# Kernel optimization log

Hardware: AMD Instinct MI355X
Metric: run time of the kernel (lower is better)

Reference implementation:

```python
import math
import jax, jax.numpy as jnp
import numpy as np

B, L, DM, H = 4, 1024, 1024, 16
D = DM // H  # head dim = 64
MAXPOS = 1024


def setup_inputs() -> dict:
    key = jax.random.key(0)
    ks = jax.random.split(key, 8)
    s = 0.02
    return {
        "hidden_states": jax.random.normal(ks[0], (B, L, DM), jnp.float32),
        "attention_mask": jnp.zeros((B, 1, 1, L), jnp.float32),
        "Wq": jax.random.normal(ks[1], (DM, DM), jnp.float32) * s,
        "bq": jax.random.normal(ks[2], (DM,), jnp.float32) * s,
        "Wk": jax.random.normal(ks[3], (DM, DM), jnp.float32) * s,
        "bk": jax.random.normal(ks[4], (DM,), jnp.float32) * s,
        "Wv": jax.random.normal(ks[5], (DM, DM), jnp.float32) * s,
        "bv": jax.random.normal(ks[6], (DM,), jnp.float32) * s,
        "dist_emb": jax.random.normal(ks[7], (2 * MAXPOS - 1, D), jnp.float32) * s,
    }


def reference(hidden_states, attention_mask, Wq, bq, Wk, bk, Wv, bv, dist_emb):
    b, l, dm = hidden_states.shape

    def split_heads(x):  # [b,l,dm] -> [b,h,l,d]
        return x.reshape(b, l, H, D).transpose(0, 2, 1, 3)

    # nn.Linear applies x @ W.T + b
    q = split_heads(hidden_states @ Wq.T + bq)
    k = split_heads(hidden_states @ Wk.T + bk)
    v = split_heads(hidden_states @ Wv.T + bv)

    scores = jnp.einsum("bhld,bhrd->bhlr", q, k)

    # relative_key_query positional bias
    pos = jnp.arange(l)
    idx = pos[:, None] - pos[None, :] + MAXPOS - 1  # [l,l] in [0, 2*MAXPOS-2]
    pe = dist_emb[idx]  # [l,l,d]
    scores = scores + jnp.einsum("bhld,lrd->bhlr", q, pe) \
                    + jnp.einsum("bhrd,lrd->bhlr", k, pe)

    scores = scores / math.sqrt(D) + attention_mask
    probs = jax.nn.softmax(scores, axis=-1)  # dropout p=0.0 -> identity

    ctx = jnp.einsum("bhlr,bhrd->bhld", probs, v)
    return ctx.transpose(0, 2, 1, 3).reshape(b, l, dm)
```

## Files before the change

### kernel.cpp

```cpp
#include <hip/hip_runtime.h>

typedef __attribute__((ext_vector_type(4))) float f32x4;
typedef __attribute__((ext_vector_type(8))) short short8;
typedef __attribute__((ext_vector_type(2))) unsigned u32x2;

typedef __attribute__((address_space(1))) const void gv_t;
typedef __attribute__((address_space(3))) void lv_t;

__device__ __forceinline__ ushort f2bf(float f) {
  union { float f; unsigned u; } v; v.f = f;
  unsigned r = v.u + 0x7fffu + ((v.u >> 16) & 1u);
  return (ushort)(r >> 16);
}
__device__ __forceinline__ float bf2f(ushort u) {
  union { unsigned u; float f; } v; v.u = ((unsigned)u) << 16;
  return v.f;
}

template<int CTRL>
__device__ __forceinline__ float dppf(float x) {
  union { float f; int i; } u; u.f = x;
  u.i = __builtin_amdgcn_update_dpp(0, u.i, CTRL, 0xf, 0xf, true);
  return u.f;
}
__device__ __forceinline__ float rmax16(float x) {
  x = fmaxf(x, dppf<0xB1>(x));
  x = fmaxf(x, dppf<0x4E>(x));
  x = fmaxf(x, dppf<0x124>(x));
  x = fmaxf(x, dppf<0x128>(x));
  return x;
}
__device__ __forceinline__ float rsum16(float x) {
  x += dppf<0xB1>(x);
  x += dppf<0x4E>(x);
  x += dppf<0x124>(x);
  x += dppf<0x128>(x);
  return x;
}

__global__ void k_prep(const float* __restrict__ hidden, const float* __restrict__ Wq,
                       const float* __restrict__ Wk, const float* __restrict__ Wv,
                       const float* __restrict__ dist, const float* __restrict__ bq,
                       const float* __restrict__ bk, const float* __restrict__ bv,
                       ushort* __restrict__ Hbf, ushort* __restrict__ Wqkv,
                       ushort* __restrict__ Ebf, float* __restrict__ Bqkv) {
  int i = blockIdx.x * blockDim.x + threadIdx.x;
  const float* src; ushort* dst; int o;
  if (i < 1048576)      { src = hidden; o = i;            dst = Hbf; }
  else if (i < 1310720) { src = Wq;   o = i - 1048576;    dst = Wqkv; }
  else if (i < 1572864) { src = Wk;   o = i - 1310720;    dst = Wqkv + 1048576; }
  else if (i < 1835008) { src = Wv;   o = i - 1572864;    dst = Wqkv + 2097152; }
  else if (i < 1867760) { src = dist; o = i - 1835008;    dst = Ebf; }
  else if (i < 1868528) {
    int ib = i - 1867760;
    const float* bs = ib < 256 ? bq : (ib < 512 ? bk : bv);
    reinterpret_cast<float4*>(Bqkv)[ib] = reinterpret_cast<const float4*>(bs)[ib & 255];
    return;
  } else return;
  float4 v = reinterpret_cast<const float4*>(src)[o];
  ushort4 u;
  u.x = f2bf(v.x); u.y = f2bf(v.y); u.z = f2bf(v.z); u.w = f2bf(v.w);
  reinterpret_cast<ushort4*>(dst)[o] = u;
}

__global__ __launch_bounds__(256) void k_gemm_qkv(
    const ushort* __restrict__ A, const ushort* __restrict__ W,
    const float* __restrict__ bias, ushort* __restrict__ C)
{
  __shared__ __align__(16) ushort As[128 * 32];
  __shared__ __align__(16) ushort Bs[128 * 32];
  const int n0 = blockIdx.x * 128;
  const int m0 = blockIdx.y * 128;
  const int tid = threadIdx.x;
  const int w = tid >> 6, lane = tid & 63;
  const int wr = (w >> 1) * 64, wc = (w & 1) * 64;
  const int lr = lane & 15, lk = (lane >> 4) * 8;

  f32x4 acc[4][4] = {};

  for (int k0 = 0; k0 < 1024; k0 += 32) {
    __syncthreads();
#pragma unroll
    for (int inst = 0; inst < 2; ++inst) {
      int chunk = w * 128 + inst * 64 + lane;
      int row = chunk >> 2, c8 = (chunk & 3) * 8;
      __builtin_amdgcn_global_load_lds(
          (gv_t*)(A + (size_t)(m0 + row) * 1024 + k0 + c8),
          (lv_t*)(As + (size_t)(w * 128 + inst * 64) * 8), 16, 0, 0);
      __builtin_amdgcn_global_load_lds(
          (gv_t*)(W + (size_t)(n0 + row) * 1024 + k0 + c8),
          (lv_t*)(Bs + (size_t)(w * 128 + inst * 64) * 8), 16, 0, 0);
    }
    __syncthreads();
    short8 af[4], bfr[4];
#pragma unroll
    for (int t = 0; t < 4; ++t) {
      af[t]  = *reinterpret_cast<const short8*>(As + (wr + t * 16 + lr) * 32 + lk);
      bfr[t] = *reinterpret_cast<const short8*>(Bs + (wc + t * 16 + lr) * 32 + lk);
    }
#pragma unroll
    for (int mt = 0; mt < 4; ++mt)
#pragma unroll
      for (int nt = 0; nt < 4; ++nt)
        acc[mt][nt] = __builtin_amdgcn_mfma_f32_16x16x32_bf16(af[mt], bfr[nt], acc[mt][nt], 0, 0, 0);
  }

  float bv[4];
#pragma unroll
  for (int nt = 0; nt < 4; ++nt) bv[nt] = bias[n0 + wc + nt * 16 + lr];
#pragma unroll
  for (int mt = 0; mt < 4; ++mt)
#pragma unroll
    for (int nt = 0; nt < 4; ++nt)
#pragma unroll
      for (int j = 0; j < 4; ++j) {
        int row = m0 + wr + mt * 16 + (lane >> 4) * 4 + j;
        int col = n0 + wc + nt * 16 + lr;
        C[(size_t)row * 3072 + col] = f2bf(acc[mt][nt][j] + bv[nt]);
      }
}

__global__ __launch_bounds__(256) void k_vt(const ushort* __restrict__ QKV,
                                            ushort* __restrict__ VT) {
  __shared__ ushort t[64][65];
  const int bh = blockIdx.y, b = bh >> 4, h = bh & 15;
  const int l0 = blockIdx.x * 64;
  const int r = threadIdx.x >> 2, c0 = (threadIdx.x & 3) * 16;
  const ushort* src = QKV + (size_t)(b * 1024 + l0 + r) * 3072 + 2048 + h * 64 + c0;
  short8 v0 = *reinterpret_cast<const short8*>(src);
  short8 v1 = *reinterpret_cast<const short8*>(src + 8);
#pragma unroll
  for (int i = 0; i < 8; ++i) {
    t[c0 + i][r] = (ushort)v0[i];
    t[c0 + 8 + i][r] = (ushort)v1[i];
  }
  __syncthreads();
  short8 o0, o1;
#pragma unroll
  for (int i = 0; i < 8; ++i) {
    o0[i] = (short)t[r][c0 + i];
    o1[i] = (short)t[r][c0 + 8 + i];
  }
  ushort* dst = VT + (size_t)(bh * 64 + r) * 1024 + l0 + c0;
  *reinterpret_cast<short8*>(dst) = o0;
  *reinterpret_cast<short8*>(dst + 8) = o1;
}

__global__ __launch_bounds__(512, 4) void k_attn(
    const ushort* __restrict__ QKV, const ushort* __restrict__ VTg,
    const ushort* __restrict__ E, const float* __restrict__ mask,
    float* __restrict__ out)
{
  __shared__ __align__(16) ushort Kl[64 * 64];
  __shared__ __align__(16) ushort Vl[64 * 64];
  __shared__ __align__(16) ushort El[256 * 64];
  __shared__ __align__(16) ushort T2s[64 * 196];

  const int lt = blockIdx.x, h = blockIdx.y, b = blockIdx.z;
  const int bh = b * 16 + h;
  const int l0 = lt * 128;
  const int tid = threadIdx.x;
  const int w = tid >> 6, lane = tid & 63;
  const int g = lane >> 4, m = lane & 15, g4 = g * 4;
  const int rsub = lane >> 3, csub = lane & 7;

  const ushort* Qg = QKV;
  const ushort* Kg = QKV + 1024;
  const float* maskrow = mask + b * 1024;

  short8 qf0, qf1;
  {
    const size_t qoff = (size_t)(b * 1024 + l0 + w * 16 + m) * 3072 + h * 64;
    qf0 = *reinterpret_cast<const short8*>(Qg + qoff + g * 8);
    qf1 = *reinterpret_cast<const short8*>(Qg + qoff + 32 + g * 8);
  }

  int srcl[4], bsel[4];
#pragma unroll
  for (int j = 0; j < 4; ++j) {
    int x = (g4 + j + 63 - m) & 15;
    srcl[j] = (lane & 48) | x;
    bsel[j] = (g4 + j) > x;
  }
  const int A0 = 195 * m + 16 * w + g4 + 63;
  const int tile0 = (w < 4) ? 2 * w : 4 + w;

  {
    int kr = w * 8 + rsub;
    __builtin_amdgcn_global_load_lds(
        (gv_t*)(Kg + (size_t)(b * 1024 + kr) * 3072 + h * 64 + ((csub ^ (kr & 7)) << 3)),
        (lv_t*)(Kl + w * 512), 16, 0, 0);
#pragma unroll
    for (int i = 0; i < 3; ++i) {
      int li = w * 3 + i;
      int er = li * 8 + rsub;
      int p = l0 + 960 + er; if (p > 2046) p = 2046;
      __builtin_amdgcn_global_load_lds(
          (gv_t*)(E + (size_t)p * 64 + ((csub ^ (er & 7)) << 3)),
          (lv_t*)(El + li * 512), 16, 0, 0);
    }
  }

  f32x4 o_[4] = {};
  float m_[4], s_[4];
#pragma unroll
  for (int j = 0; j < 4; ++j) { m_[j] = -1e30f; s_[j] = 0.f; }

  int rot = 0;

  for (int rt = 0; rt < 16; ++rt) {
    const int r0 = rt * 64;
    __syncthreads();

    {
      int dr = w * 8 + rsub;
      __builtin_amdgcn_global_load_lds(
          (gv_t*)(VTg + (size_t)(bh * 64 + dr) * 1024 + r0 + ((csub ^ (dr & 7)) << 3)),
          (lv_t*)(Vl + w * 512), 16, 0, 0);
    }

    short8 ea0[2], ea1[2];
    {
      int row = tile0 * 16 + m, phys = (row + rot) & 255;
      ea0[0] = *reinterpret_cast<const short8*>(El + phys * 64 + ((g ^ (row & 7)) << 3));
      ea0[1] = *reinterpret_cast<const short8*>(El + phys * 64 + (((g + 4) ^ (row & 7)) << 3));
    }
    if (w < 4) {
      int row = (tile0 + 1) * 16 + m, phys = (row + rot) & 255;
      ea1[0] = *reinterpret_cast<const short8*>(El + phys * 64 + ((g ^ (row & 7)) << 3));
      ea1[1] = *reinterpret_cast<const short8*>(El + phys * 64 + (((g + 4) ^ (row & 7)) << 3));
    }

    f32x4 sc[4];
#pragma unroll
    for (int ft = 0; ft < 4; ++ft) {
      int kr = ft * 16 + m;
      short8 kb0 = *reinterpret_cast<const short8*>(Kl + kr * 64 + ((g ^ (kr & 7)) << 3));
      short8 kb1 = *reinterpret_cast<const short8*>(Kl + kr * 64 + (((g + 4) ^ (kr & 7)) << 3));
      f32x4 z = {0.f, 0.f, 0.f, 0.f};
      sc[ft] = __builtin_amdgcn_mfma_f32_16x16x32_bf16(qf1, kb1,
               __builtin_amdgcn_mfma_f32_16x16x32_bf16(qf0, kb0, z, 0, 0, 0), 0, 0, 0);
      {
        f32x4 t2 = __builtin_amdgcn_mfma_f32_16x16x32_bf16(ea0[1], kb1,
                   __builtin_amdgcn_mfma_f32_16x16x32_bf16(ea0[0], kb0, z, 0, 0, 0), 0, 0, 0);
        u32x2 pk;
        pk[0] = (unsigned)f2bf(t2[0]) | ((unsigned)f2bf(t2[1]) << 16);
        pk[1] = (unsigned)f2bf(t2[2]) | ((unsigned)f2bf(t2[3]) << 16);
        *reinterpret_cast<u32x2*>(T2s + (ft * 16 + m) * 196 + tile0 * 16 + g4) = pk;
      }
      if (w < 4) {
        f32x4 t2 = __builtin_amdgcn_mfma_f32_16x16x32_bf16(ea1[1], kb1,
                   __builtin_amdgcn_mfma_f32_16x16x32_bf16(ea1[0], kb0, z, 0, 0, 0), 0, 0, 0);
        u32x2 pk;
        pk[0] = (unsigned)f2bf(t2[0]) | ((unsigned)f2bf(t2[1]) << 16);
        pk[1] = (unsigned)f2bf(t2[2]) | ((unsigned)f2bf(t2[3]) << 16);
        *reinterpret_cast<u32x2*>(T2s + (ft * 16 + m) * 196 + (tile0 + 1) * 16 + g4) = pk;
      }
    }

    f32x4 t1loc[5];
#pragma unroll
    for (int lti = 0; lti < 5; ++lti) {
      int row = (w + lti) * 16 + m, phys = (row + rot) & 255;
      short8 e0 = *reinterpret_cast<const short8*>(El + phys * 64 + ((g ^ (row & 7)) << 3));
      short8 e1 = *reinterpret_cast<const short8*>(El + phys * 64 + (((g + 4) ^ (row & 7)) << 3));
      f32x4 z = {0.f, 0.f, 0.f, 0.f};
      t1loc[lti] = __builtin_amdgcn_mfma_f32_16x16x32_bf16(qf1, e1,
                   __builtin_amdgcn_mfma_f32_16x16x32_bf16(qf0, e0, z, 0, 0, 0), 0, 0, 0);
    }

    __syncthreads();

    if (rt < 15) {
      int kr = w * 8 + rsub;
      __builtin_amdgcn_global_load_lds(
          (gv_t*)(Kg + (size_t)(b * 1024 + r0 + 64 + kr) * 3072 + h * 64 + ((csub ^ (kr & 7)) << 3)),
          (lv_t*)(Kl + w * 512), 16, 0, 0);
      int X = (rot + 192) & 255;
      int er = w * 8 + rsub;
      int p = l0 + 960 - 64 * (rt + 1) + er;
      __builtin_amdgcn_global_load_lds(
          (gv_t*)(E + (size_t)p * 64 + ((csub ^ (er & 7)) << 3)),
          (lv_t*)(El + (X + w * 8) * 64), 16, 0, 0);
    }

    float sv[4][4];
#pragma unroll
    for (int ct = 0; ct < 4; ++ct) {
      float mk = maskrow[r0 + ct * 16 + m];
#pragma unroll
      for (int j = 0; j < 4; ++j) {
        float t2v = bf2f(T2s[A0 + 3120 * ct + j]);
        float val = bsel[j] ? t1loc[4 - ct][j] : t1loc[3 - ct][j];
        float t1v = __shfl(val, srcl[j]);
        sv[ct][j] = (sc[ct][j] + t1v + t2v) * 0.125f + mk;
      }
    }

#pragma unroll
    for (int j = 0; j < 4; ++j) {
      float rm = fmaxf(fmaxf(sv[0][j], sv[1][j]), fmaxf(sv[2][j], sv[3][j]));
      rm = rmax16(rm);
      float mn = fmaxf(m_[j], rm);
      float al = __expf(m_[j] - mn);
      float rs = 0.f;
#pragma unroll
      for (int ct = 0; ct < 4; ++ct) {
        float p = __expf(sv[ct][j] - mn);
        sv[ct][j] = p; rs += p;
      }
      rs = rsum16(rs);
      s_[j] = s_[j] * al + rs;
      m_[j] = mn;
#pragma unroll
      for (int vt = 0; vt < 4; ++vt) o_[vt][j] *= al;
    }

    __syncthreads();

    ushort* Pp = (ushort*)T2s;
#pragma unroll
    for (int ct = 0; ct < 4; ++ct)
#pragma unroll
      for (int j = 0; j < 4; ++j) {
        int e = g4 + j;
        int f = ct * 16 + m;
        Pp[w * 1024 + e * 64 + ((((f >> 3) ^ (e & 7)) << 3) | (f & 7))] = f2bf(sv[ct][j]);
      }

    {
      short8 pf0 = *reinterpret_cast<const short8*>(Pp + w * 1024 + m * 64 + ((g ^ (m & 7)) << 3));
      short8 pf1 = *reinterpret_cast<const short8*>(Pp + w * 1024 + m * 64 + (((g + 4) ^ (m & 7)) << 3));
#pragma unroll
      for (int vt = 0; vt < 4; ++vt) {
        int dr = vt * 16 + m;
        short8 vb0 = *reinterpret_cast<const short8*>(Vl + dr * 64 + ((g ^ (dr & 7)) << 3));
        short8 vb1 = *reinterpret_cast<const short8*>(Vl + dr * 64 + (((g + 4) ^ (dr & 7)) << 3));
        o_[vt] = __builtin_amdgcn_mfma_f32_16x16x32_bf16(pf0, vb0, o_[vt], 0, 0, 0);
        o_[vt] = __builtin_amdgcn_mfma_f32_16x16x32_bf16(pf1, vb1, o_[vt], 0, 0, 0);
      }
    }

    rot = (rot + 192) & 255;
  }

#pragma unroll
  for (int j = 0; j < 4; ++j) {
    float inv = 1.0f / s_[j];
    int row = b * 1024 + l0 + w * 16 + g4 + j;
#pragma unroll
    for (int vt = 0; vt < 4; ++vt)
      out[(size_t)row * 1024 + h * 64 + vt * 16 + m] = o_[vt][j] * inv;
  }
}

extern "C" void kernel_launch(void* const* d_in, const int* in_sizes, int n_in,
                              void* d_out, int out_size, void* d_ws, size_t ws_size,
                              hipStream_t stream) {
  const float* hidden = (const float*)d_in[0];
  const float* mask   = (const float*)d_in[1];
  const float* Wq = (const float*)d_in[2];
  const float* bq = (const float*)d_in[3];
  const float* Wk = (const float*)d_in[4];
  const float* bk = (const float*)d_in[5];
  const float* Wv = (const float*)d_in[6];
  const float* bv = (const float*)d_in[7];
  const float* dist = (const float*)d_in[8];
  float* out = (float*)d_out;

  char* ws = (char*)d_ws;
  ushort* Hbf  = (ushort*)(ws);
  ushort* Wqkv = (ushort*)(ws + 8388608);
  float*  Bqkv = (float*) (ws + 8388608 + 6291456);
  ushort* Ebf  = (ushort*)(ws + 8388608 + 6291456 + 16384);
  ushort* QKV  = (ushort*)(ws + 8388608 + 6291456 + 16384 + 262144);
  ushort* VT   = Hbf;

  k_prep<<<7299, 256, 0, stream>>>(hidden, Wq, Wk, Wv, dist, bq, bk, bv,
                                   Hbf, Wqkv, Ebf, Bqkv);
  k_gemm_qkv<<<dim3(24, 32), 256, 0, stream>>>(Hbf, Wqkv, Bqkv, QKV);
  k_vt<<<dim3(16, 64), 256, 0, stream>>>(QKV, VT);
  k_attn<<<dim3(8, 16, 4), 512, 0, stream>>>(QKV, VT, Ebf, mask, out);
}
```

Before: 163.1 us.

## Swizzle block order, shrink E ring buffer, dedicate P buffer, add setprio around MFMAs

```diff
diff --git a/kernel.cpp b/kernel.cpp
--- a/kernel.cpp
+++ b/kernel.cpp
@@ -69,8 +69,10 @@
 {
   __shared__ __align__(16) ushort As[128 * 32];
   __shared__ __align__(16) ushort Bs[128 * 32];
-  const int n0 = blockIdx.x * 128;
-  const int m0 = blockIdx.y * 128;
+  int linear = blockIdx.x + blockIdx.y * 24;
+  int swzb = (linear & 7) * 96 + (linear >> 3);
+  const int n0 = (swzb % 24) * 128;
+  const int m0 = (swzb / 24) * 128;
   const int tid = threadIdx.x;
   const int w = tid >> 6, lane = tid & 63;
   const int wr = (w >> 1) * 64, wc = (w & 1) * 64;
@@ -153,10 +155,14 @@
 {
   __shared__ __align__(16) ushort Kl[64 * 64];
   __shared__ __align__(16) ushort Vl[64 * 64];
-  __shared__ __align__(16) ushort El[256 * 64];
-  __shared__ __align__(16) ushort T2s[64 * 196];
-
-  const int lt = blockIdx.x, h = blockIdx.y, b = blockIdx.z;
+  __shared__ __align__(16) ushort El[192 * 64];
+  __shared__ __align__(16) ushort T2s[64 * 192];
+  __shared__ __align__(16) ushort Pp[8 * 1024];
+
+  int linear = blockIdx.x + (blockIdx.y << 3) + (blockIdx.z << 7);
+  int swzb = (linear & 7) * 64 + (linear >> 3);
+  const int lt = swzb & 7, h = (swzb >> 3) & 15, b = swzb >> 7;
+
   const int bh = b * 16 + h;
   const int l0 = lt * 128;
   const int tid = threadIdx.x;
@@ -182,7 +188,7 @@
     srcl[j] = (lane & 48) | x;
     bsel[j] = (g4 + j) > x;
   }
-  const int A0 = 195 * m + 16 * w + g4 + 63;
+  const int A0 = 191 * m + 16 * w + g4 + 63;
   const int tile0 = (w < 4) ? 2 * w : 4 + w;
 
   {
@@ -221,15 +227,19 @@
 
     short8 ea0[2], ea1[2];
     {
-      int row = tile0 * 16 + m, phys = (row + rot) & 255;
-      ea0[0] = *reinterpret_cast<const short8*>(El + phys * 64 + ((g ^ (row & 7)) << 3));
-      ea0[1] = *reinterpret_cast<const short8*>(El + phys * 64 + (((g + 4) ^ (row & 7)) << 3));
+      int row = tile0 * 16 + m;
+      int x = row + rot; if (x >= 192) x -= 192;
+      ea0[0] = *reinterpret_cast<const short8*>(El + x * 64 + ((g ^ (row & 7)) << 3));
+      ea0[1] = *reinterpret_cast<const short8*>(El + x * 64 + (((g + 4) ^ (row & 7)) << 3));
     }
     if (w < 4) {
-      int row = (tile0 + 1) * 16 + m, phys = (row + rot) & 255;
-      ea1[0] = *reinterpret_cast<const short8*>(El + phys * 64 + ((g ^ (row & 7)) << 3));
-      ea1[1] = *reinterpret_cast<const short8*>(El + phys * 64 + (((g + 4) ^ (row & 7)) << 3));
-    }
+      int row = (tile0 + 1) * 16 + m;
+      int x = row + rot; if (x >= 192) x -= 192;
+      ea1[0] = *reinterpret_cast<const short8*>(El + x * 64 + ((g ^ (row & 7)) << 3));
+      ea1[1] = *reinterpret_cast<const short8*>(El + x * 64 + (((g + 4) ^ (row & 7)) << 3));
+    }
+
+    __builtin_amdgcn_s_setprio(1);
 
     f32x4 sc[4];
 #pragma unroll
@@ -246,7 +256,7 @@
         u32x2 pk;
         pk[0] = (unsigned)f2bf(t2[0]) | ((unsigned)f2bf(t2[1]) << 16);
         pk[1] = (unsigned)f2bf(t2[2]) | ((unsigned)f2bf(t2[3]) << 16);
-        *reinterpret_cast<u32x2*>(T2s + (ft * 16 + m) * 196 + tile0 * 16 + g4) = pk;
+        *reinterpret_cast<u32x2*>(T2s + (ft * 16 + m) * 192 + tile0 * 16 + g4) = pk;
       }
       if (w < 4) {
         f32x4 t2 = __builtin_amdgcn_mfma_f32_16x16x32_bf16(ea1[1], kb1,
@@ -254,21 +264,24 @@
         u32x2 pk;
         pk[0] = (unsigned)f2bf(t2[0]) | ((unsigned)f2bf(t2[1]) << 16);
         pk[1] = (unsigned)f2bf(t2[2]) | ((unsigned)f2bf(t2[3]) << 16);
-        *reinterpret_cast<u32x2*>(T2s + (ft * 16 + m) * 196 + (tile0 + 1) * 16 + g4) = pk;
+        *reinterpret_cast<u32x2*>(T2s + (ft * 16 + m) * 192 + (tile0 + 1) * 16 + g4) = pk;
       }
     }
 
     f32x4 t1loc[5];
 #pragma unroll
     for (int lti = 0; lti < 5; ++lti) {
-      int row = (w + lti) * 16 + m, phys = (row + rot) & 255;
-      short8 e0 = *reinterpret_cast<const short8*>(El + phys * 64 + ((g ^ (row & 7)) << 3));
-      short8 e1 = *reinterpret_cast<const short8*>(El + phys * 64 + (((g + 4) ^ (row & 7)) << 3));
+      int row = (w + lti) * 16 + m;
+      int x = row + rot; if (x >= 192) x -= 192;
+      short8 e0 = *reinterpret_cast<const short8*>(El + x * 64 + ((g ^ (row & 7)) << 3));
+      short8 e1 = *reinterpret_cast<const short8*>(El + x * 64 + (((g + 4) ^ (row & 7)) << 3));
       f32x4 z = {0.f, 0.f, 0.f, 0.f};
       t1loc[lti] = __builtin_amdgcn_mfma_f32_16x16x32_bf16(qf1, e1,
                    __builtin_amdgcn_mfma_f32_16x16x32_bf16(qf0, e0, z, 0, 0, 0), 0, 0, 0);
     }
 
+    __builtin_amdgcn_s_setprio(0);
+
     __syncthreads();
 
     if (rt < 15) {
@@ -276,7 +289,7 @@
       __builtin_amdgcn_global_load_lds(
           (gv_t*)(Kg + (size_t)(b * 1024 + r0 + 64 + kr) * 3072 + h * 64 + ((csub ^ (kr & 7)) << 3)),
           (lv_t*)(Kl + w * 512), 16, 0, 0);
-      int X = (rot + 192) & 255;
+      int X = rot + 128; if (X >= 192) X -= 192;
       int er = w * 8 + rsub;
       int p = l0 + 960 - 64 * (rt + 1) + er;
       __builtin_amdgcn_global_load_lds(
@@ -290,7 +303,7 @@
       float mk = maskrow[r0 + ct * 16 + m];
 #pragma unroll
       for (int j = 0; j < 4; ++j) {
-        float t2v = bf2f(T2s[A0 + 3120 * ct + j]);
+        float t2v = bf2f(T2s[A0 + 3056 * ct + j]);
         float val = bsel[j] ? t1loc[4 - ct][j] : t1loc[3 - ct][j];
         float t1v = __shfl(val, srcl[j]);
         sv[ct][j] = (sc[ct][j] + t1v + t2v) * 0.125f + mk;
@@ -316,9 +329,6 @@
       for (int vt = 0; vt < 4; ++vt) o_[vt][j] *= al;
     }
 
-    __syncthreads();
-
-    ushort* Pp = (ushort*)T2s;
 #pragma unroll
     for (int ct = 0; ct < 4; ++ct)
 #pragma unroll
@@ -331,6 +341,7 @@
     {
       short8 pf0 = *reinterpret_cast<const short8*>(Pp + w * 1024 + m * 64 + ((g ^ (m & 7)) << 3));
       short8 pf1 = *reinterpret_cast<const short8*>(Pp + w * 1024 + m * 64 + (((g + 4) ^ (m & 7)) << 3));
+      __builtin_amdgcn_s_setprio(1);
 #pragma unroll
       for (int vt = 0; vt < 4; ++vt) {
         int dr = vt * 16 + m;
@@ -339,9 +350,10 @@
         o_[vt] = __builtin_amdgcn_mfma_f32_16x16x32_bf16(pf0, vb0, o_[vt], 0, 0, 0);
         o_[vt] = __builtin_amdgcn_mfma_f32_16x16x32_bf16(pf1, vb1, o_[vt], 0, 0, 0);
       }
-    }
-
-    rot = (rot + 192) & 255;
+      __builtin_amdgcn_s_setprio(0);
+    }
+
+    rot -= 64; if (rot < 0) rot += 192;
   }
 
 #pragma unroll
```

Result: slower. 179.8 us, median of 2 (+10.2%).
